# Kernel tuning notes

Hardware: AMD Instinct MI355X
Metric: run time of the kernel (lower is better)

## Reference

```python
import jax, jax.numpy as jnp
import numpy as np

CLASSES = 80
COORDS = 4
NUM = 5
LEN_PER_ANCHOR = COORDS + 1 + CLASSES  # 85


def setup_inputs() -> dict:
    key = jax.random.key(0)
    x = jax.random.normal(key, (16, NUM * LEN_PER_ANCHOR, 76, 76), dtype=jnp.float32)
    return {"x": x}


def reference(x) -> jnp.ndarray:
    B, C, H, W = x.shape
    # [B, num, len_per_anchor, H, W]
    v = x.reshape(B, NUM, LEN_PER_ANCHOR, H, W)
    xy = jax.nn.sigmoid(v[:, :, 0:2])            # tx, ty
    obj = jax.nn.sigmoid(v[:, :, 4:5])           # objectness
    cls = jax.nn.softmax(v[:, :, 5:], axis=2)    # class probs over 80 classes
    # Note: channels 2,3 (raw w,h) are dropped, matching the torch module.
    out = jnp.concatenate([xy, obj, cls], axis=2)  # [B, num, 3+classes, H, W]
    return out.reshape(B, NUM * (3 + CLASSES), H, W)
```

## Files before the change

kernel.cpp:

```cpp
#include <hip/hip_runtime.h>
#include <hip/hip_bf16.h>
#include <math.h>

#define BATCH 16
#define NUMA 5
#define LPA 85
#define OUTC 83
#define HW (76 * 76)
#define CLS 80

__device__ __forceinline__ float fast_sigmoid(float v) {
    float e = __expf(-v);
    return __frcp_rn(1.0f + e);
}

__global__ __launch_bounds__(256) void region_kernel(
        const float* __restrict__ x, float* __restrict__ out) {
    const int idx = blockIdx.x * blockDim.x + threadIdx.x;
    const int total = BATCH * NUMA * HW;
    if (idx >= total) return;

    const int hw = idx % HW;
    const int bn = idx / HW;

    const float* __restrict__ px = x + (size_t)bn * LPA * HW + hw;
    float* __restrict__ po = out + (size_t)bn * OUTC * HW + hw;

    const float v_x = px[0 * HW];
    const float v_y = px[1 * HW];
    const float v_o = px[4 * HW];

    float cls[CLS];
    #pragma unroll
    for (int c = 0; c < CLS; ++c) {
        cls[c] = px[(5 + c) * HW];
    }

    float m = cls[0];
    #pragma unroll
    for (int c = 1; c < CLS; ++c) m = fmaxf(m, cls[c]);

    float sum = 0.0f;
    #pragma unroll
    for (int c = 0; c < CLS; ++c) {
        float e = __expf(cls[c] - m);
        cls[c] = e;
        sum += e;
    }
    const float inv = __frcp_rn(sum);

    po[0 * HW] = fast_sigmoid(v_x);
    po[1 * HW] = fast_sigmoid(v_y);
    po[2 * HW] = fast_sigmoid(v_o);
    #pragma unroll
    for (int c = 0; c < CLS; ++c) {
        po[(3 + c) * HW] = cls[c] * inv;
    }
}

extern "C" void kernel_launch(void* const* d_in, const int* in_sizes, int n_in,
                              void* d_out, int out_size, void* d_ws, size_t ws_size,
                              hipStream_t stream) {
    const float* x = (const float*)d_in[0];
    float* out = (float*)d_out;

    const int total = BATCH * NUMA * HW;
    const int block = 256;
    const int grid = (total + block - 1) / block;

    region_kernel<<<grid, block, 0, stream>>>(x, out);
}
```

Baseline: 270.4 us.

## Split class softmax across half-waves and drop max subtraction

Each spatial position is now handled by two threads in different half-waves. Each thread loads and exponentiates 40 of the 80 classes, and the partial sums are combined with a cross-half shuffle. The max subtraction pass is removed and the launch bounds request higher occupancy. This halves per-thread register use and doubles thread-level parallelism to hide memory latency. The trade-offs are overflow risk for large logits and smaller contiguous runs per wave access.

```diff
diff --git a/kernel.cpp b/kernel.cpp
--- a/kernel.cpp
+++ b/kernel.cpp
@@ -7,54 +7,58 @@
 #define LPA 85
 #define OUTC 83
 #define HW (76 * 76)
-#define CLS 80
+#define TOTALP (BATCH * NUMA * HW)
+#define CHALF 40
 
 __device__ __forceinline__ float fast_sigmoid(float v) {
     float e = __expf(-v);
     return __frcp_rn(1.0f + e);
 }
 
-__global__ __launch_bounds__(256) void region_kernel(
+__global__ __launch_bounds__(256, 8) void region_kernel(
         const float* __restrict__ x, float* __restrict__ out) {
-    const int idx = blockIdx.x * blockDim.x + threadIdx.x;
-    const int total = BATCH * NUMA * HW;
-    if (idx >= total) return;
+    const int tid  = blockIdx.x * 256 + threadIdx.x;
+    const int lane = tid & 63;
+    const int wave = tid >> 6;
+    const int h    = lane >> 5;
+    const int li   = lane & 31;
+    const int P    = wave * 32 + li;
+    const int hw   = P % HW;
+    const int bn   = P / HW;
 
-    const int hw = idx % HW;
-    const int bn = idx / HW;
+    const float* __restrict__ px = x   + (size_t)bn * (LPA * HW) + hw;
+    float* __restrict__       po = out + (size_t)bn * (OUTC * HW) + hw;
 
-    const float* __restrict__ px = x + (size_t)bn * LPA * HW + hw;
-    float* __restrict__ po = out + (size_t)bn * OUTC * HW + hw;
+    const float va = px[(h == 0 ? 0 : 4) * HW];
+    const float vb = px[(h == 0 ? 1 : 4) * HW];
 
-    const float v_x = px[0 * HW];
-    const float v_y = px[1 * HW];
-    const float v_o = px[4 * HW];
+    const int cbase = 5 + h * CHALF;
+    float cls[CHALF];
+    #pragma unroll
+    for (int c = 0; c < CHALF; ++c) cls[c] = px[(cbase + c) * HW];
 
-    float cls[CLS];
+    float s0 = 0.f, s1 = 0.f;
     #pragma unroll
-    for (int c = 0; c < CLS; ++c) {
-        cls[c] = px[(5 + c) * HW];
+    for (int c = 0; c < CHALF; c += 2) {
+        float e0 = __expf(cls[c]);
+        float e1 = __expf(cls[c + 1]);
+        cls[c] = e0; cls[c + 1] = e1;
+        s0 += e0; s1 += e1;
     }
+    const float psum = s0 + s1;
+    const float total = psum + __shfl_xor(psum, 32, 64);
+    const float inv = __frcp_rn(total);
 
-    float m = cls[0];
+    if (h == 0) {
+        po[0 * HW] = fast_sigmoid(va);
+        po[1 * HW] = fast_sigmoid(vb);
+    } else {
+        po[2 * HW] = fast_sigmoid(va);
+    }
+    const int obase = 3 + h * CHALF;
     #pragma unroll
-    for (int c = 1; c < CLS; ++c) m = fmaxf(m, cls[c]);
-
-    float sum = 0.0f;
-    #pragma unroll
-    for (int c = 0; c < CLS; ++c) {
-        float e = __expf(cls[c] - m);
-        cls[c] = e;
-        sum += e;
-    }
-    const float inv = __frcp_rn(sum);
-
-    po[0 * HW] = fast_sigmoid(v_x);
-    po[1 * HW] = fast_sigmoid(v_y);
-    po[2 * HW] = fast_sigmoid(v_o);
-    #pragma unroll
-    for (int c = 0; c < CLS; ++c) {
-        po[(3 + c) * HW] = cls[c] * inv;
+    for (int c = 0; c < CHALF; ++c) {
+        po[(obase + c) * HW] = cls[c] * inv;
     }
 }
 
@@ -64,9 +68,9 @@
     const float* x = (const float*)d_in[0];
     float* out = (float*)d_out;
 
-    const int total = BATCH * NUMA * HW;
+    const int total_threads = TOTALP * 2;
     const int block = 256;
-    const int grid = (total + block - 1) / block;
+    const int grid = total_threads / block;
 
     region_kernel<<<grid, block, 0, stream>>>(x, out);
 }
```

New measurement: 277.7 us. 1.03x slower.
